# Kernel optimization log

Hardware: AMD Instinct MI355X
Metric: run time of the kernel (lower is better)

Reference implementation:

```python
import jax, jax.numpy as jnp
import numpy as np

N = 20000   # nodes
E = 256000  # edges
G = 64      # graphs
EPS = 1e-5  # batchnorm eps


def setup_inputs() -> dict:
    key = jax.random.key(0)
    ks = jax.random.split(key, 20)
    inp = {}
    inp['x'] = jax.random.normal(ks[0], (N, 6), dtype=jnp.float32)
    inp['edge_index'] = jax.random.randint(ks[1], (2, E), 0, N)
    inp['batch'] = jnp.sort(jax.random.randint(ks[2], (N,), 0, G))
    conv_dims = [(6, 32), (32, 64), (64, 128), (128, 1024)]
    ki = 3
    for li, (a, b) in enumerate(conv_dims, 1):
        inp[f'W{li}'] = jax.random.normal(ks[ki], (a, b), dtype=jnp.float32) / np.sqrt(a).astype(np.float32); ki += 1
        inp[f'b{li}'] = jnp.zeros((b,), jnp.float32)
        inp[f'g{li}'] = jnp.ones((b,), jnp.float32)
        inp[f'be{li}'] = jnp.zeros((b,), jnp.float32)
    fc_dims = [(1024, 512), (512, 256), (256, 64)]
    for li, (a, b) in enumerate(fc_dims, 5):
        inp[f'W{li}'] = jax.random.normal(ks[ki], (a, b), dtype=jnp.float32) / np.sqrt(a).astype(np.float32); ki += 1
        inp[f'b{li}'] = jnp.zeros((b,), jnp.float32)
        if li < 7:
            inp[f'g{li}'] = jnp.ones((b,), jnp.float32)
            inp[f'be{li}'] = jnp.zeros((b,), jnp.float32)
    return inp


def _bn(h, g, be):
    # training-mode BatchNorm1d: biased variance over dim 0
    m = h.mean(axis=0)
    v = h.var(axis=0)
    return g * (h - m) * jax.lax.rsqrt(v + EPS) + be


def reference(x, edge_index, batch,
              W1, b1, g1, be1, W2, b2, g2, be2,
              W3, b3, g3, be3, W4, b4, g4, be4,
              W5, b5, g5, be5, W6, b6, g6, be6,
              W7, b7):
    loops = jnp.arange(N)
    src = jnp.concatenate([edge_index[0], loops])  # [E+N], message sources
    dst = jnp.concatenate([edge_index[1], loops])  # [E+N], aggregation targets
    deg = jax.ops.segment_sum(jnp.ones(E + N, x.dtype), dst, num_segments=N)
    dinv = jax.lax.rsqrt(deg)                      # deg >= 1 (self-loops)
    norm = dinv[src] * dinv[dst]                   # symmetric GCN normalization

    def gcn(h, W, b):
        h = h @ W                                   # [N, out]
        agg = jax.ops.segment_sum(norm[:, None] * h[src], dst, num_segments=N)
        return agg + b

    h = jax.nn.relu(_bn(gcn(x, W1, b1), g1, be1))
    h = jax.nn.relu(_bn(gcn(h, W2, b2), g2, be2))
    h = jax.nn.relu(_bn(gcn(h, W3, b3), g3, be3))
    h = jax.nn.relu(_bn(gcn(h, W4, b4), g4, be4))
    p = jax.ops.segment_max(h, batch, num_segments=G)  # global max pool [G, 1024]
    p = jax.nn.relu(_bn(p @ W5 + b5, g5, be5))
    p = jax.nn.relu(_bn(p @ W6 + b6, g6, be6))
    y = p @ W7 + b7
    n = jnp.maximum(jnp.linalg.norm(y, axis=1, keepdims=True), 1e-12)
    return y / n
```

## Files before the change

### kernel.cpp

```cpp
#include <hip/hip_runtime.h>
#include <math.h>

#define NN 20000
#define EE 256000
#define GG 64
#define CDIV(a,b) (((a)+(b)-1)/(b))
#define RB4 157

typedef __attribute__((ext_vector_type(8))) short bf16x8;
typedef __attribute__((ext_vector_type(4))) float f32x4;

__device__ __forceinline__ unsigned fkey(float f) {
  unsigned u = __float_as_uint(f);
  return (u & 0x80000000u) ? ~u : (u | 0x80000000u);
}
__device__ __forceinline__ float fdec(unsigned k) {
  unsigned u = (k & 0x80000000u) ? (k ^ 0x80000000u) : ~k;
  return __uint_as_float(u);
}
__device__ __forceinline__ unsigned short rne_bf16(float f) {
  unsigned u = __float_as_uint(f);
  unsigned r = (u + 0x7fffu + ((u >> 16) & 1u)) >> 16;
  return (unsigned short)r;
}


__global__ void k_prep(int* deg) {
  int i = blockIdx.x*blockDim.x + threadIdx.x;
  if (i < NN) deg[i] = 1;
}

__global__ void k_deg(const int* __restrict__ dst, int* deg) {
  int i = blockIdx.x*blockDim.x + threadIdx.x;
  if (i < EE) atomicAdd(&deg[dst[i]], 1);
}

__global__ __launch_bounds__(256) void k_scan_bsum(const int* __restrict__ deg,
                                                   int* __restrict__ bsum) {
  __shared__ int red[256];
  int b = blockIdx.x, t = threadIdx.x;
  int idx = b*1024 + t*4;
  int4 v = make_int4(0,0,0,0);
  if (idx < NN) v = *(const int4*)&deg[idx];
  red[t] = v.x + v.y + v.z + v.w;
  __syncthreads();
  for (int off = 128; off > 0; off >>= 1) {
    if (t < off) red[t] += red[t+off];
    __syncthreads();
  }
  if (t == 0) bsum[b] = red[0];
}

__global__ __launch_bounds__(256) void k_scan_apply(
    const int* __restrict__ deg, const int* __restrict__ bsum,
    int* __restrict__ offsets, int* __restrict__ cursor, float* __restrict__ dinv) {
  __shared__ int base_s;
  __shared__ int tsum[256];
  int b = blockIdx.x, t = threadIdx.x;
  if (t == 0) {
    int s = 0;
    for (int i = 0; i < b; ++i) s += bsum[i];
    base_s = s;
  }
  int idx = b*1024 + t*4;
  int4 v = make_int4(0,0,0,0);
  if (idx < NN) v = *(const int4*)&deg[idx];
  tsum[t] = v.x + v.y + v.z + v.w;
  __syncthreads();
  for (int off = 1; off < 256; off <<= 1) {
    int u = (t >= off) ? tsum[t-off] : 0;
    __syncthreads();
    tsum[t] += u;
    __syncthreads();
  }
  int excl = (t == 0) ? 0 : tsum[t-1];
  if (idx < NN) {
    int base = base_s + excl;
    int o0 = base;
    int o1 = o0 + v.x;
    int o2 = o1 + v.y;
    int o3 = o2 + v.z;
    *(int4*)&offsets[idx] = make_int4(o0,o1,o2,o3);
    *(int4*)&cursor[idx]  = make_int4(o0,o1,o2,o3);
    float4 dv;
    dv.x = rsqrtf((float)v.x); dv.y = rsqrtf((float)v.y);
    dv.z = rsqrtf((float)v.z); dv.w = rsqrtf((float)v.w);
    *(float4*)&dinv[idx] = dv;
    if (idx + 4 == NN) offsets[NN] = o3 + v.w;
  }
}

__global__ void k_fill(const int* __restrict__ srcv, const int* __restrict__ dstv,
                       const float* __restrict__ dinv, int* cursor,
                       int* __restrict__ csr_src, float* __restrict__ csr_w) {
  int i = blockIdx.x*blockDim.x + threadIdx.x;
  if (i < EE) {
    int s = srcv[i], d = dstv[i];
    int pos = atomicAdd(&cursor[d], 1);
    csr_src[pos] = s;
    csr_w[pos] = dinv[s] * dinv[d];
  } else if (i < EE + NN) {
    int n = i - EE;
    int pos = atomicAdd(&cursor[n], 1);
    csr_src[pos] = n;
    float di = dinv[n];
    csr_w[pos] = di * di;
  }
}


template<int C, int TX, int TY>
__global__ void k_agg(const float* __restrict__ in, const int* __restrict__ offsets,
                      const int* __restrict__ csr_src, const float* __restrict__ csr_w,
                      float* __restrict__ out) {
  int node = blockIdx.x * TY + threadIdx.y;
  if (node >= NN) return;
  int x = threadIdx.x;
  int k0 = offsets[node], k1 = offsets[node+1];
  if (x < C) {
    float acc = 0.f;
    for (int k = k0; k < k1; ++k) {
      int s = csr_src[k];
      float w = csr_w[k];
      acc += w * in[s*C + x];
    }
    out[node*C + x] = acc;
  }
}

template<int C, int TY>
__global__ void k_agg_f4(const float* __restrict__ in, const float* __restrict__ st,
                         const float* __restrict__ g, const float* __restrict__ be,
                         const int* __restrict__ offsets, const int* __restrict__ csr_src,
                         const float* __restrict__ csr_w, float* __restrict__ out) {
  int node = blockIdx.x*TY + threadIdx.y;
  if (node >= NN) return;
  int c0 = threadIdx.x*4;
  float4 mean = *(const float4*)&st[c0];
  float4 rstd = *(const float4*)&st[C+c0];
  float4 gv = *(const float4*)&g[c0];
  float4 bv = *(const float4*)&be[c0];
  float sx = gv.x*rstd.x, hx = bv.x - mean.x*sx;
  float sy = gv.y*rstd.y, hy = bv.y - mean.y*sy;
  float sz = gv.z*rstd.z, hz = bv.z - mean.z*sz;
  float sw = gv.w*rstd.w, hw = bv.w - mean.w*sw;
  int k0 = offsets[node], k1 = offsets[node+1];
  float p0=0.f,p1=0.f,p2=0.f,p3=0.f;
  float q0=0.f,q1=0.f,q2=0.f,q3=0.f;
  int k = k0;
  for (; k + 2 <= k1; k += 2) {
    int s0 = csr_src[k], s1 = csr_src[k+1];
    float w0 = csr_w[k], w1 = csr_w[k+1];
    float4 u = *(const float4*)&in[s0*C + c0];
    float4 v = *(const float4*)&in[s1*C + c0];
    p0 += w0*fmaxf(u.x*sx+hx, 0.f);
    p1 += w0*fmaxf(u.y*sy+hy, 0.f);
    p2 += w0*fmaxf(u.z*sz+hz, 0.f);
    p3 += w0*fmaxf(u.w*sw+hw, 0.f);
    q0 += w1*fmaxf(v.x*sx+hx, 0.f);
    q1 += w1*fmaxf(v.y*sy+hy, 0.f);
    q2 += w1*fmaxf(v.z*sz+hz, 0.f);
    q3 += w1*fmaxf(v.w*sw+hw, 0.f);
  }
  if (k < k1) {
    int s0 = csr_src[k]; float w0 = csr_w[k];
    float4 u = *(const float4*)&in[s0*C + c0];
    p0 += w0*fmaxf(u.x*sx+hx, 0.f);
    p1 += w0*fmaxf(u.y*sy+hy, 0.f);
    p2 += w0*fmaxf(u.z*sz+hz, 0.f);
    p3 += w0*fmaxf(u.w*sw+hw, 0.f);
  }
  *(float4*)&out[node*C+c0] = make_float4(p0+q0, p1+q1, p2+q2, p3+q3);
}

__global__ void k_agg_bf_f4(const float* __restrict__ in, const float* __restrict__ st,
                            const float* __restrict__ g, const float* __restrict__ be,
                            const int* __restrict__ offsets, const int* __restrict__ csr_src,
                            const float* __restrict__ csr_w, unsigned short* __restrict__ out) {
  int node = blockIdx.x*8 + threadIdx.y;
  if (node >= NN) return;
  int c0 = threadIdx.x*4;
  float4 mean = *(const float4*)&st[c0];
  float4 rstd = *(const float4*)&st[128+c0];
  float4 gv = *(const float4*)&g[c0];
  float4 bv = *(const float4*)&be[c0];
  float sx = gv.x*rstd.x, hx = bv.x - mean.x*sx;
  float sy = gv.y*rstd.y, hy = bv.y - mean.y*sy;
  float sz = gv.z*rstd.z, hz = bv.z - mean.z*sz;
  float sw = gv.w*rstd.w, hw = bv.w - mean.w*sw;
  int k0 = offsets[node], k1 = offsets[node+1];
  float p0=0.f,p1=0.f,p2=0.f,p3=0.f;
  float q0=0.f,q1=0.f,q2=0.f,q3=0.f;
  int k = k0;
  for (; k + 2 <= k1; k += 2) {
    int s0 = csr_src[k], s1 = csr_src[k+1];
    float w0 = csr_w[k], w1 = csr_w[k+1];
    float4 u = *(const float4*)&in[s0*128 + c0];
    float4 v = *(const float4*)&in[s1*128 + c0];
    p0 += w0*fmaxf(u.x*sx+hx, 0.f);
    p1 += w0*fmaxf(u.y*sy+hy, 0.f);
    p2 += w0*fmaxf(u.z*sz+hz, 0.f);
    p3 += w0*fmaxf(u.w*sw+hw, 0.f);
    q0 += w1*fmaxf(v.x*sx+hx, 0.f);
    q1 += w1*fmaxf(v.y*sy+hy, 0.f);
    q2 += w1*fmaxf(v.z*sz+hz, 0.f);
    q3 += w1*fmaxf(v.w*sw+hw, 0.f);
  }
  if (k < k1) {
    int s0 = csr_src[k]; float w0 = csr_w[k];
    float4 u = *(const float4*)&in[s0*128 + c0];
    p0 += w0*fmaxf(u.x*sx+hx, 0.f);
    p1 += w0*fmaxf(u.y*sy+hy, 0.f);
    p2 += w0*fmaxf(u.z*sz+hz, 0.f);
    p3 += w0*fmaxf(u.w*sw+hw, 0.f);
  }
  ushort4 o;
  o.x = rne_bf16(p0+q0); o.y = rne_bf16(p1+q1);
  o.z = rne_bf16(p2+q2); o.w = rne_bf16(p3+q3);
  *(ushort4*)&out[node*128 + c0] = o;
}

__global__ void k_wprep(const float* __restrict__ W, unsigned short* __restrict__ out) {
  int i = blockIdx.x*256 + threadIdx.x;
  if (i >= 128*1024) return;
  int k = i >> 10, c = i & 1023;
  out[c*128 + k] = rne_bf16(W[i]);
}


template<int K, int OUT, int ROWS>
__global__ __launch_bounds__(256) void k_gemm_small(
    const float* __restrict__ A, const float* __restrict__ W,
    float* __restrict__ out, float* __restrict__ pstats) {
  constexpr int RG  = 256 / OUT;
  constexpr int RPT = ROWS / RG;
  __shared__ float Ws[K*OUT];
  __shared__ float As[ROWS*K];
  __shared__ float reds[2][RG][OUT];
  int t = threadIdx.x;
  for (int i = t; i < K*OUT; i += 256) Ws[i] = W[i];
  int row0 = blockIdx.x * ROWS;
  for (int i = t; i < ROWS*K; i += 256) As[i] = A[row0*K + i];
  __syncthreads();
  int j  = t % OUT;
  int rg = t / OUT;
  float acc[RPT] = {};
  for (int k = 0; k < K; ++k) {
    float w = Ws[k*OUT + j];
    #pragma unroll
    for (int i = 0; i < RPT; ++i)
      acc[i] += As[(rg*RPT + i)*K + k] * w;
  }
  float s = 0.f, ss = 0.f;
  #pragma unroll
  for (int i = 0; i < RPT; ++i) {
    out[(row0 + rg*RPT + i)*OUT + j] = acc[i];
    s += acc[i]; ss += acc[i]*acc[i];
  }
  reds[0][rg][j] = s; reds[1][rg][j] = ss;
  __syncthreads();
  if (rg == 0) {
    float S = 0.f, SS = 0.f;
    #pragma unroll
    for (int r = 0; r < RG; ++r) { S += reds[0][r][j]; SS += reds[1][r][j]; }
    int p = blockIdx.x & 15;
    atomicAdd(&pstats[p*2*OUT + j], S);
    atomicAdd(&pstats[p*2*OUT + OUT + j], SS);
  }
}

template<int C>
__global__ void k_finalize_ps(const float* __restrict__ pstats, float* __restrict__ stats) {
  int c = blockIdx.x*64 + threadIdx.x;
  if (c >= C) return;
  float s = 0.f, ss = 0.f;
  #pragma unroll
  for (int p = 0; p < 16; ++p) { s += pstats[p*2*C + c]; ss += pstats[p*2*C + C + c]; }
  float m = s * (1.f/NN);
  float v = ss * (1.f/NN) - m*m;
  stats[c] = m;
  stats[C+c] = rsqrtf(v + 1e-5f);
}


__global__ __launch_bounds__(256) void k_gemm_l4_mfma(
    const unsigned short* __restrict__ A, const unsigned short* __restrict__ Bt,
    const int* __restrict__ batch,
    float* __restrict__ ps4, unsigned* __restrict__ pmax, unsigned* __restrict__ pmin) {
  __shared__ unsigned short As[128*128];
  __shared__ unsigned short Bs[128*128];
  __shared__ float scr_s[512];
  __shared__ float scr_p[512];
  int t = threadIdx.x;
  int row0 = blockIdx.x * 128;
  #pragma unroll
  for (int j = 0; j < 8; ++j) {
    int c = j*256 + t;
    int r = c >> 4, ck = c & 15;
    int rg = row0 + r;
    ulonglong2 v; v.x = 0; v.y = 0;
    if (rg < NN) v = *(const ulonglong2*)&A[(size_t)rg*128 + ck*8];
    *(ulonglong2*)&As[r*128 + (ck ^ (r & 7))*8] = v;
  }
  int w = t >> 6, l = t & 63;
  int wr = w >> 1, wc = w & 1;
  int lrow = l & 15, lk = l >> 4;
  int rbase = row0 + wr*64;
  int rlast_b = min(row0 + 127, NN - 1);
  int glo_b = batch[row0], ghi_b = batch[rlast_b];
  bool block_same = (glo_b == ghi_b);

  for (int p = 0; p < 2; ++p) {
    int col0 = (blockIdx.y*2 + p)*128;
    if (p) __syncthreads();
    #pragma unroll
    for (int j = 0; j < 8; ++j) {
      int c = j*256 + t;
      int r = c >> 4, ck = c & 15;
      ulonglong2 v = *(const ulonglong2*)&Bt[(size_t)(col0 + r)*128 + ck*8];
      *(ulonglong2*)&Bs[r*128 + (ck ^ (r & 7))*8] = v;
    }
    __syncthreads();

    f32x4 acc[4][4] = {};
    #pragma unroll
    for (int ks = 0; ks < 4; ++ks) {
      int kc = ks*4 + lk;
      bf16x8 a[4], b[4];
      #pragma unroll
      for (int m = 0; m < 4; ++m) {
        int r = wr*64 + m*16 + lrow;
        a[m] = *(const bf16x8*)&As[r*128 + (kc ^ (r & 7))*8];
      }
      #pragma unroll
      for (int n = 0; n < 4; ++n) {
        int r = wc*64 + n*16 + lrow;
        b[n] = *(const bf16x8*)&Bs[r*128 + (kc ^ (r & 7))*8];
      }
      #pragma unroll
      for (int m = 0; m < 4; ++m)
        #pragma unroll
        for (int n = 0; n < 4; ++n)
          acc[m][n] = __builtin_amdgcn_mfma_f32_16x16x32_bf16(a[m], b[n], acc[m][n], 0, 0, 0);
    }

    float s[4] = {}, ss[4] = {};
    float mx[4], mn[4];
    #pragma unroll
    for (int n = 0; n < 4; ++n) { mx[n] = -3.4e38f; mn[n] = 3.4e38f; }
    #pragma unroll
    for (int m = 0; m < 4; ++m)
      #pragma unroll
      for (int r = 0; r < 4; ++r) {
        int row_g = rbase + m*16 + lk*4 + r;
        if (row_g < NN) {
          #pragma unroll
          for (int n = 0; n < 4; ++n) {
            float v = acc[m][n][r];
            s[n] += v; ss[n] += v*v;
            mx[n] = fmaxf(mx[n], v); mn[n] = fminf(mn[n], v);
          }
        }
      }
    #pragma unroll
    for (int n = 0; n < 4; ++n) {
      s[n]  += __shfl_xor(s[n], 16);  s[n]  += __shfl_xor(s[n], 32);
      ss[n] += __shfl_xor(ss[n], 16); ss[n] += __shfl_xor(ss[n], 32);
    }
    if (block_same) {
      #pragma unroll
      for (int n = 0; n < 4; ++n) {
        mx[n] = fmaxf(mx[n], __shfl_xor(mx[n], 16)); mx[n] = fmaxf(mx[n], __shfl_xor(mx[n], 32));
        mn[n] = fminf(mn[n], __shfl_xor(mn[n], 16)); mn[n] = fminf(mn[n], __shfl_xor(mn[n], 32));
      }
    }
    if (l < 16) {
      #pragma unroll
      for (int n = 0; n < 4; ++n) {
        int si = (((wr*2 + wc)*4 + n)*16 + l)*2;
        scr_s[si]   = s[n];
        scr_s[si+1] = ss[n];
        if (block_same) { scr_p[si] = mx[n]; scr_p[si+1] = mn[n]; }
      }
    }
    __syncthreads();
    if (wr == 0 && l < 16) {
      #pragma unroll
      for (int n = 0; n < 4; ++n) {
        int si0 = (((0*2 + wc)*4 + n)*16 + l)*2;
        int si1 = (((1*2 + wc)*4 + n)*16 + l)*2;
        int cg  = col0 + wc*64 + n*16 + l;
        ps4[(size_t)blockIdx.x*2048 + cg]        = scr_s[si0]   + scr_s[si1];
        ps4[(size_t)blockIdx.x*2048 + 1024 + cg] = scr_s[si0+1] + scr_s[si1+1];
        if (block_same) {
          float bmx = fmaxf(scr_p[si0],   scr_p[si1]);
          float bmn = fminf(scr_p[si0+1], scr_p[si1+1]);
          if (bmx > -3.0e38f) atomicMax(&pmax[glo_b*1024 + cg], fkey(bmx));
          if (bmn <  3.0e38f) atomicMin(&pmin[glo_b*1024 + cg], fkey(bmn));
        }
      }
    }
    if (!block_same && rbase < NN) {
      int rlast = min(rbase + 63, NN - 1);
      int glo = batch[rbase], ghi = batch[rlast];
      if (glo == ghi) {
        #pragma unroll
        for (int n = 0; n < 4; ++n) {
          mx[n] = fmaxf(mx[n], __shfl_xor(mx[n], 16)); mx[n] = fmaxf(mx[n], __shfl_xor(mx[n], 32));
          mn[n] = fminf(mn[n], __shfl_xor(mn[n], 16)); mn[n] = fminf(mn[n], __shfl_xor(mn[n], 32));
        }
        if (l < 16) {
          #pragma unroll
          for (int n = 0; n < 4; ++n) {
            int cg = col0 + wc*64 + n*16 + l;
            atomicMax(&pmax[glo*1024 + cg], fkey(mx[n]));
            atomicMin(&pmin[glo*1024 + cg], fkey(mn[n]));
          }
        }
      } else {
        int gb[4][4];
        #pragma unroll
        for (int m = 0; m < 4; ++m)
          #pragma unroll
          for (int r = 0; r < 4; ++r) {
            int row_g = rbase + m*16 + lk*4 + r;
            gb[m][r] = (row_g < NN) ? batch[row_g] : -1;
          }
        for (int g = glo; g <= ghi; ++g) {
          float gmx[4], gmn[4];
          #pragma unroll
          for (int n = 0; n < 4; ++n) { gmx[n] = -3.4e38f; gmn[n] = 3.4e38f; }
          #pragma unroll
          for (int m = 0; m < 4; ++m)
            #pragma unroll
            for (int r = 0; r < 4; ++r) {
              bool in_g = (gb[m][r] == g);
              #pragma unroll
              for (int n = 0; n < 4; ++n) {
                float v = acc[m][n][r];
                gmx[n] = in_g ? fmaxf(gmx[n], v) : gmx[n];
                gmn[n] = in_g ? fminf(gmn[n], v) : gmn[n];
              }
            }
          #pragma unroll
          for (int n = 0; n < 4; ++n) {
            gmx[n] = fmaxf(gmx[n], __shfl_xor(gmx[n], 16)); gmx[n] = fmaxf(gmx[n], __shfl_xor(gmx[n], 32));
            gmn[n] = fminf(gmn[n], __shfl_xor(gmn[n], 16)); gmn[n] = fminf(gmn[n], __shfl_xor(gmn[n], 32));
          }
          if (l < 16) {
            #pragma unroll
            for (int n = 0; n < 4; ++n) {
              int cg = col0 + wc*64 + n*16 + l;
              if (gmx[n] > -3.0e38f) atomicMax(&pmax[g*1024 + cg], fkey(gmx[n]));
              if (gmn[n] <  3.0e38f) atomicMin(&pmin[g*1024 + cg], fkey(gmn[n]));
            }
          }
        }
      }
    }
  }
}

__global__ void k_finalize_l4(const float* __restrict__ ps4, float* __restrict__ stats) {
  int c = blockIdx.x*256 + threadIdx.x;
  float s = 0.f, ss = 0.f;
  #pragma unroll 8
  for (int rb = 0; rb < RB4; ++rb) {
    s  += ps4[(size_t)rb*2048 + c];
    ss += ps4[(size_t)rb*2048 + 1024 + c];
  }
  float m = s * (1.f/NN);
  float v = ss * (1.f/NN) - m*m;
  stats[c] = m;
  stats[1024 + c] = rsqrtf(v + 1e-5f);
}

__global__ void k_bnpool(const unsigned* __restrict__ pmax, const unsigned* __restrict__ pmin,
                         const float* __restrict__ stats, const float* __restrict__ g,
                         const float* __restrict__ be, float* __restrict__ p) {
  int i = blockIdx.x*256 + threadIdx.x;
  if (i >= 64*1024) return;
  int c = i & 1023;
  float mean = stats[c], rstd = stats[1024+c];
  float sc = g[c]*rstd, sh = be[c] - mean*sc;
  float v = (sc >= 0.f) ? fdec(pmax[i]) : fdec(pmin[i]);
  p[i] = fmaxf(v*sc + sh, 0.f);
}


template<int K, int OUT, int KT>
__global__ __launch_bounds__(256) void k_fc_tile(
    const float* __restrict__ A, const float* __restrict__ W,
    float* __restrict__ out) {
  __shared__ float As[64][KT];
  __shared__ float Ws[KT][64];
  int t = threadIdx.y*64 + threadIdx.x;
  int j0 = blockIdx.x*64;
  int k0 = blockIdx.y*KT;
  #pragma unroll 4
  for (int i = t; i < 64*KT/4; i += 256) {
    int r  = i / (KT/4);
    int c4 = i % (KT/4);
    float4 v = *(const float4*)&A[r*K + k0 + c4*4];
    *(float4*)&As[r][c4*4] = v;
  }
  #pragma unroll 4
  for (int i = t; i < KT*16; i += 256) {
    int k  = i / 16;
    int c4 = i % 16;
    float4 v = *(const float4*)&W[(k0+k)*OUT + j0 + c4*4];
    *(float4*)&Ws[k][c4*4] = v;
  }
  __syncthreads();
  int j  = threadIdx.x;
  int r0 = threadIdx.y*16;
  float acc[16] = {};
  for (int kk = 0; kk < KT; ++kk) {
    float w = Ws[kk][j];
    #pragma unroll
    for (int i = 0; i < 16; ++i) acc[i] += As[r0+i][kk] * w;
  }
  #pragma unroll
  for (int i = 0; i < 16; ++i) atomicAdd(&out[(r0+i)*OUT + j0 + j], acc[i]);
}

__global__ __launch_bounds__(512) void k_bn_rows(
    float* __restrict__ h, const float* __restrict__ g,
    const float* __restrict__ be, int C) {
  int c = blockIdx.x*64 + threadIdx.x;
  int y = threadIdx.y;
  float v[8];
  float s = 0.f, ss = 0.f;
  #pragma unroll
  for (int i = 0; i < 8; ++i) {
    v[i] = h[(y*8+i)*C + c];
    s += v[i]; ss += v[i]*v[i];
  }
  __shared__ float rs[8][64], rss[8][64], bc[2][64];
  rs[y][threadIdx.x] = s; rss[y][threadIdx.x] = ss;
  __syncthreads();
  if (y == 0) {
    s = 0.f; ss = 0.f;
    #pragma unroll
    for (int i = 0; i < 8; ++i) { s += rs[i][threadIdx.x]; ss += rss[i][threadIdx.x]; }
    float m = s*(1.f/64.f);
    float var = ss*(1.f/64.f) - m*m;
    float rstd = rsqrtf(var + 1e-5f);
    float sc = g[c]*rstd;
    bc[0][threadIdx.x] = sc;
    bc[1][threadIdx.x] = be[c] - m*sc;
  }
  __syncthreads();
  float sc = bc[0][threadIdx.x], sh = bc[1][threadIdx.x];
  #pragma unroll
  for (int i = 0; i < 8; ++i)
    h[(y*8+i)*C + c] = fmaxf(v[i]*sc + sh, 0.f);
}

__global__ void k_l2norm(const float* __restrict__ in, const float* __restrict__ b,
                         float* __restrict__ out) {
  int r = blockIdx.x, j = threadIdx.x;
  float v = in[r*64 + j] + b[j];
  float ss = v*v;
  #pragma unroll
  for (int off = 1; off < 64; off <<= 1) ss += __shfl_xor(ss, off);
  float inv = 1.f / fmaxf(sqrtf(ss), 1e-12f);
  out[r*64 + j] = v * inv;
}


extern "C" void kernel_launch(void* const* d_in, const int* in_sizes, int n_in,
                              void* d_out, int out_size, void* d_ws, size_t ws_size,
                              hipStream_t stream) {
  const float* x    = (const float*)d_in[0];
  const int*   ei   = (const int*)d_in[1];
  const int*   batch= (const int*)d_in[2];
  const float* W1=(const float*)d_in[3],  *g1=(const float*)d_in[5],  *be1=(const float*)d_in[6];
  const float* W2=(const float*)d_in[7],  *g2=(const float*)d_in[9],  *be2=(const float*)d_in[10];
  const float* W3=(const float*)d_in[11], *g3=(const float*)d_in[13], *be3=(const float*)d_in[14];
  const float* W4=(const float*)d_in[15], *g4=(const float*)d_in[17], *be4=(const float*)d_in[18];
  const float* W5=(const float*)d_in[19], *g5=(const float*)d_in[21], *be5=(const float*)d_in[22];
  const float* W6=(const float*)d_in[23], *g6=(const float*)d_in[25], *be6=(const float*)d_in[26];
  const float* W7=(const float*)d_in[27], *b7=(const float*)d_in[28];
  const int* esrc = ei;
  const int* edst = ei + EE;

  char* w = (char*)d_ws;
  auto alloc = [&](size_t bytes) -> void* {
    void* p = (void*)w;
    w += (bytes + 255) & ~(size_t)255;
    return p;
  };
  int*   deg     = (int*)  alloc(NN*4);
  int*   offsets = (int*)  alloc((NN+1)*4);
  int*   cursor  = (int*)  alloc(NN*4);
  int*   bsum    = (int*)  alloc(32*4);
  float* dinv    = (float*)alloc(NN*4);
  int*   csr_src = (int*)  alloc((EE+NN)*4);
  float* csr_w   = (float*)alloc((EE+NN)*4);
  float* stats1  = (float*)alloc(2*32*4);
  float* stats2  = (float*)alloc(2*64*4);
  float* stats3  = (float*)alloc(2*128*4);
  float* stats4  = (float*)alloc(2*1024*4);
  float* pstats  = (float*)alloc(16*2*128*4);
  float* ps4     = (float*)alloc((size_t)RB4*2048*4);
  float* agg     = (float*)alloc((size_t)NN*128*4);
  float* hbufA   = (float*)alloc((size_t)NN*128*4);
  float* hbufB   = (float*)alloc((size_t)NN*64*4);
  float* pooled  = (float*)alloc(64*1024*4);
  float* fc1     = (float*)alloc(64*512*4);
  float* fc2     = (float*)alloc(64*256*4);
  float* fc3raw  = (float*)alloc(64*64*4);
  unsigned short* agg_bf = (unsigned short*)alloc((size_t)NN*128*2);
  unsigned short* wt_bf  = (unsigned short*)alloc(1024*128*2);
  unsigned* pmax = (unsigned*)alloc(64*1024*4);
  unsigned* pmin = (unsigned*)alloc(64*1024*4);

  k_prep<<<CDIV(NN,256),256,0,stream>>>(deg);
  k_deg<<<CDIV(EE,256),256,0,stream>>>(edst, deg);
  k_scan_bsum<<<20,256,0,stream>>>(deg, bsum);
  k_scan_apply<<<20,256,0,stream>>>(deg, bsum, offsets, cursor, dinv);
  k_fill<<<CDIV(EE+NN,256),256,0,stream>>>(esrc, edst, dinv, cursor, csr_src, csr_w);

  k_agg<6,8,32><<<CDIV(NN,32),dim3(8,32),0,stream>>>(x, offsets, csr_src, csr_w, agg);
  hipMemsetAsync(pstats, 0, 16*2*32*4, stream);
  k_gemm_small<6,32,32><<<NN/32,256,0,stream>>>(agg, W1, hbufA, pstats);
  k_finalize_ps<32><<<1,64,0,stream>>>(pstats, stats1);

  k_agg_f4<32,32><<<CDIV(NN,32),dim3(8,32),0,stream>>>(hbufA, stats1, g1, be1, offsets, csr_src, csr_w, agg);
  hipMemsetAsync(pstats, 0, 16*2*64*4, stream);
  k_gemm_small<32,64,16><<<NN/16,256,0,stream>>>(agg, W2, hbufB, pstats);
  k_finalize_ps<64><<<1,64,0,stream>>>(pstats, stats2);

  k_agg_f4<64,16><<<CDIV(NN,16),dim3(16,16),0,stream>>>(hbufB, stats2, g2, be2, offsets, csr_src, csr_w, agg);
  hipMemsetAsync(pstats, 0, 16*2*128*4, stream);
  k_gemm_small<64,128,16><<<NN/16,256,0,stream>>>(agg, W3, hbufA, pstats);
  k_finalize_ps<128><<<2,64,0,stream>>>(pstats, stats3);

  k_agg_bf_f4<<<CDIV(NN,8),dim3(32,8),0,stream>>>(hbufA, stats3, g3, be3, offsets, csr_src, csr_w, agg_bf);
  k_wprep<<<CDIV(128*1024,256),256,0,stream>>>(W4, wt_bf);
  hipMemsetAsync(pmax, 0x00, 64*1024*4, stream);
  hipMemsetAsync(pmin, 0xFF, 64*1024*4, stream);
  k_gemm_l4_mfma<<<dim3(RB4,4),256,0,stream>>>(agg_bf, wt_bf, batch, ps4, pmax, pmin);
  k_finalize_l4<<<4,256,0,stream>>>(ps4, stats4);
  k_bnpool<<<CDIV(64*1024,256),256,0,stream>>>(pmax, pmin, stats4, g4, be4, pooled);

  hipMemsetAsync(fc1, 0, 64*512*4, stream);
  k_fc_tile<1024,512,128><<<dim3(8,8),dim3(64,4),0,stream>>>(pooled, W5, fc1);
  k_bn_rows<<<8,dim3(64,8),0,stream>>>(fc1, g5, be5, 512);

  hipMemsetAsync(fc2, 0, 64*256*4, stream);
  k_fc_tile<512,256,128><<<dim3(4,4),dim3(64,4),0,stream>>>(fc1, W6, fc2);
  k_bn_rows<<<4,dim3(64,8),0,stream>>>(fc2, g6, be6, 256);

  hipMemsetAsync(fc3raw, 0, 64*64*4, stream);
  k_fc_tile<256,64,64><<<dim3(1,4),dim3(64,4),0,stream>>>(fc2, W7, fc3raw);
  k_l2norm<<<64,64,0,stream>>>(fc3raw, b7, (float*)d_out);
}
```

Before: 337.3 us.

## Fold memsets into neighboring kernels, fuse finalize with pooling, widen L4 column loop

Replaces every hipMemsetAsync with zeroing done inside the preceding kernel (aggregation, bf16 aggregation, finalize, bn_rows), removing several small launches from the stream. Merges the layer-4 stats finalize and the BN+max-pool kernel into one kernel that also zeroes fc1. Halves the layer-4 MFMA grid's y dimension so each block processes four 128-column panels, reusing the staged A tile more but with fewer blocks in flight. The finalize kernel now runs only 4 blocks looping over 64 graphs, which gives less parallelism for that step.

```diff
diff --git a/kernel.cpp b/kernel.cpp
--- a/kernel.cpp
+++ b/kernel.cpp
@@ -112,7 +112,11 @@
 template<int C, int TX, int TY>
 __global__ void k_agg(const float* __restrict__ in, const int* __restrict__ offsets,
                       const int* __restrict__ csr_src, const float* __restrict__ csr_w,
-                      float* __restrict__ out) {
+                      float* __restrict__ out, float* __restrict__ pz, int pzn) {
+  if (blockIdx.x == 0) {
+    int tt = threadIdx.y*TX + threadIdx.x;
+    for (int i = tt; i < pzn; i += TX*TY) pz[i] = 0.f;
+  }
   int node = blockIdx.x * TY + threadIdx.y;
   if (node >= NN) return;
   int x = threadIdx.x;
@@ -128,11 +132,16 @@
   }
 }
 
-template<int C, int TY>
+template<int C, int TX, int TY>
 __global__ void k_agg_f4(const float* __restrict__ in, const float* __restrict__ st,
                          const float* __restrict__ g, const float* __restrict__ be,
                          const int* __restrict__ offsets, const int* __restrict__ csr_src,
-                         const float* __restrict__ csr_w, float* __restrict__ out) {
+                         const float* __restrict__ csr_w, float* __restrict__ out,
+                         float* __restrict__ pz, int pzn) {
+  if (blockIdx.x == 0) {
+    int tt = threadIdx.y*TX + threadIdx.x;
+    for (int i = tt; i < pzn; i += TX*TY) pz[i] = 0.f;
+  }
   int node = blockIdx.x*TY + threadIdx.y;
   if (node >= NN) return;
   int c0 = threadIdx.x*4;
@@ -176,7 +185,12 @@
 __global__ void k_agg_bf_f4(const float* __restrict__ in, const float* __restrict__ st,
                             const float* __restrict__ g, const float* __restrict__ be,
                             const int* __restrict__ offsets, const int* __restrict__ csr_src,
-                            const float* __restrict__ csr_w, unsigned short* __restrict__ out) {
+                            const float* __restrict__ csr_w, unsigned short* __restrict__ out,
+                            unsigned* __restrict__ pmax, unsigned* __restrict__ pmin) {
+  {
+    int idx = blockIdx.x*256 + threadIdx.y*32 + threadIdx.x;
+    if (idx < 64*1024) { pmax[idx] = 0u; pmin[idx] = 0xFFFFFFFFu; }
+  }
   int node = blockIdx.x*8 + threadIdx.y;
   if (node >= NN) return;
   int c0 = threadIdx.x*4;
@@ -310,8 +324,8 @@
   int glo_b = batch[row0], ghi_b = batch[rlast_b];
   bool block_same = (glo_b == ghi_b);
 
-  for (int p = 0; p < 2; ++p) {
-    int col0 = (blockIdx.y*2 + p)*128;
+  for (int p = 0; p < 4; ++p) {
+    int col0 = (blockIdx.y*4 + p)*128;
     if (p) __syncthreads();
     #pragma unroll
     for (int j = 0; j < 8; ++j) {
@@ -461,7 +475,11 @@
   }
 }
 
-__global__ void k_finalize_l4(const float* __restrict__ ps4, float* __restrict__ stats) {
+__global__ void k_finalize_l4_pool(const float* __restrict__ ps4,
+                                   const unsigned* __restrict__ pmax,
+                                   const unsigned* __restrict__ pmin,
+                                   const float* __restrict__ g, const float* __restrict__ be,
+                                   float* __restrict__ pooled, float* __restrict__ fc1z) {
   int c = blockIdx.x*256 + threadIdx.x;
   float s = 0.f, ss = 0.f;
   #pragma unroll 8
@@ -470,21 +488,15 @@
     ss += ps4[(size_t)rb*2048 + 1024 + c];
   }
   float m = s * (1.f/NN);
-  float v = ss * (1.f/NN) - m*m;
-  stats[c] = m;
-  stats[1024 + c] = rsqrtf(v + 1e-5f);
-}
-
-__global__ void k_bnpool(const unsigned* __restrict__ pmax, const unsigned* __restrict__ pmin,
-                         const float* __restrict__ stats, const float* __restrict__ g,
-                         const float* __restrict__ be, float* __restrict__ p) {
-  int i = blockIdx.x*256 + threadIdx.x;
-  if (i >= 64*1024) return;
-  int c = i & 1023;
-  float mean = stats[c], rstd = stats[1024+c];
-  float sc = g[c]*rstd, sh = be[c] - mean*sc;
-  float v = (sc >= 0.f) ? fdec(pmax[i]) : fdec(pmin[i]);
-  p[i] = fmaxf(v*sc + sh, 0.f);
+  float var = ss * (1.f/NN) - m*m;
+  float rstd = rsqrtf(var + 1e-5f);
+  float sc = g[c]*rstd, sh = be[c] - m*sc;
+  bool use_max = (sc >= 0.f);
+  for (int gph = 0; gph < GG; ++gph) {
+    unsigned key = use_max ? pmax[gph*1024 + c] : pmin[gph*1024 + c];
+    pooled[gph*1024 + c] = fmaxf(fdec(key)*sc + sh, 0.f);
+  }
+  for (int i = c; i < 64*512; i += 1024) fc1z[i] = 0.f;
 }
 
 
@@ -526,9 +538,15 @@
 
 __global__ __launch_bounds__(512) void k_bn_rows(
     float* __restrict__ h, const float* __restrict__ g,
-    const float* __restrict__ be, int C) {
+    const float* __restrict__ be, int C,
+    float* __restrict__ zbuf, int zn) {
   int c = blockIdx.x*64 + threadIdx.x;
   int y = threadIdx.y;
+  {
+    int tid = (blockIdx.x*8 + y)*64 + threadIdx.x;
+    int nth = gridDim.x*512;
+    for (int i = tid; i < zn; i += nth) zbuf[i] = 0.f;
+  }
   float v[8];
   float s = 0.f, ss = 0.f;
   #pragma unroll
@@ -601,7 +619,6 @@
   float* stats1  = (float*)alloc(2*32*4);
   float* stats2  = (float*)alloc(2*64*4);
   float* stats3  = (float*)alloc(2*128*4);
-  float* stats4  = (float*)alloc(2*1024*4);
   float* pstats  = (float*)alloc(16*2*128*4);
   float* ps4     = (float*)alloc((size_t)RB4*2048*4);
   float* agg     = (float*)alloc((size_t)NN*128*4);
@@ -622,38 +639,27 @@
   k_scan_apply<<<20,256,0,stream>>>(deg, bsum, offsets, cursor, dinv);
   k_fill<<<CDIV(EE+NN,256),256,0,stream>>>(esrc, edst, dinv, cursor, csr_src, csr_w);
 
-  k_agg<6,8,32><<<CDIV(NN,32),dim3(8,32),0,stream>>>(x, offsets, csr_src, csr_w, agg);
-  hipMemsetAsync(pstats, 0, 16*2*32*4, stream);
+  k_agg<6,8,32><<<CDIV(NN,32),dim3(8,32),0,stream>>>(x, offsets, csr_src, csr_w, agg, pstats, 16*2*32);
   k_gemm_small<6,32,32><<<NN/32,256,0,stream>>>(agg, W1, hbufA, pstats);
   k_finalize_ps<32><<<1,64,0,stream>>>(pstats, stats1);
 
-  k_agg_f4<32,32><<<CDIV(NN,32),dim3(8,32),0,stream>>>(hbufA, stats1, g1, be1, offsets, csr_src, csr_w, agg);
-  hipMemsetAsync(pstats, 0, 16*2*64*4, stream);
+  k_agg_f4<32,8,32><<<CDIV(NN,32),dim3(8,32),0,stream>>>(hbufA, stats1, g1, be1, offsets, csr_src, csr_w, agg, pstats, 16*2*64);
   k_gemm_small<32,64,16><<<NN/16,256,0,stream>>>(agg, W2, hbufB, pstats);
   k_finalize_ps<64><<<1,64,0,stream>>>(pstats, stats2);
 
-  k_agg_f4<64,16><<<CDIV(NN,16),dim3(16,16),0,stream>>>(hbufB, stats2, g2, be2, offsets, csr_src, csr_w, agg);
-  hipMemsetAsync(pstats, 0, 16*2*128*4, stream);
+  k_agg_f4<64,16,16><<<CDIV(NN,16),dim3(16,16),0,stream>>>(hbufB, stats2, g2, be2, offsets, csr_src, csr_w, agg, pstats, 16*2*128);
   k_gemm_small<64,128,16><<<NN/16,256,0,stream>>>(agg, W3, hbufA, pstats);
   k_finalize_ps<128><<<2,64,0,stream>>>(pstats, stats3);
 
-  k_agg_bf_f4<<<CDIV(NN,8),dim3(32,8),0,stream>>>(hbufA, stats3, g3, be3, offsets, csr_src, csr_w, agg_bf);
+  k_agg_bf_f4<<<CDIV(NN,8),dim3(32,8),0,stream>>>(hbufA, stats3, g3, be3, offsets, csr_src, csr_w, agg_bf, pmax, pmin);
   k_wprep<<<CDIV(128*1024,256),256,0,stream>>>(W4, wt_bf);
-  hipMemsetAsync(pmax, 0x00, 64*1024*4, stream);
-  hipMemsetAsync(pmin, 0xFF, 64*1024*4, stream);
-  k_gemm_l4_mfma<<<dim3(RB4,4),256,0,stream>>>(agg_bf, wt_bf, batch, ps4, pmax, pmin);
-  k_finalize_l4<<<4,256,0,stream>>>(ps4, stats4);
-  k_bnpool<<<CDIV(64*1024,256),256,0,stream>>>(pmax, pmin, stats4, g4, be4, pooled);
-
-  hipMemsetAsync(fc1, 0, 64*512*4, stream);
+  k_gemm_l4_mfma<<<dim3(RB4,2),256,0,stream>>>(agg_bf, wt_bf, batch, ps4, pmax, pmin);
+  k_finalize_l4_pool<<<4,256,0,stream>>>(ps4, pmax, pmin, g4, be4, pooled, fc1);
+
   k_fc_tile<1024,512,128><<<dim3(8,8),dim3(64,4),0,stream>>>(pooled, W5, fc1);
-  k_bn_rows<<<8,dim3(64,8),0,stream>>>(fc1, g5, be5, 512);
-
-  hipMemsetAsync(fc2, 0, 64*256*4, stream);
+  k_bn_rows<<<8,dim3(64,8),0,stream>>>(fc1, g5, be5, 512, fc2, 64*256);
   k_fc_tile<512,256,128><<<dim3(4,4),dim3(64,4),0,stream>>>(fc1, W6, fc2);
-  k_bn_rows<<<4,dim3(64,8),0,stream>>>(fc2, g6, be6, 256);
-
-  hipMemsetAsync(fc3raw, 0, 64*64*4, stream);
+  k_bn_rows<<<4,dim3(64,8),0,stream>>>(fc2, g6, be6, 256, fc3raw, 64*64);
   k_fc_tile<256,64,64><<<dim3(1,4),dim3(64,4),0,stream>>>(fc2, W7, fc3raw);
   k_l2norm<<<64,64,0,stream>>>(fc3raw, b7, (float*)d_out);
 }
```

Result: no change. 338.1 us (+0.2%).
